# Performance work log

Hardware: AMD Instinct MI355X
Metric: run time of the kernel (lower is better)

Reference implementation:

```python
import jax, jax.numpy as jnp
import numpy as np

TOP_K = 2


def setup_inputs() -> dict:
    key = jax.random.key(0)
    ks = jax.random.split(key, 5)
    B, S, D, F, E = 2, 2048, 1024, 3584, 8
    scale_in = 1.0 / np.sqrt(D)
    scale_f = 1.0 / np.sqrt(F)
    return {
        "hidden_states": jax.random.normal(ks[0], (B, S, D), dtype=jnp.float32),
        "gate_w": jax.random.normal(ks[1], (E, D), dtype=jnp.float32) * scale_in,
        "w1": jax.random.normal(ks[2], (E, F, D), dtype=jnp.float32) * scale_in,
        "w3": jax.random.normal(ks[3], (E, F, D), dtype=jnp.float32) * scale_in,
        "w2": jax.random.normal(ks[4], (E, D, F), dtype=jnp.float32) * scale_f,
    }


def _routing_weights(logits):
    # softmax over experts, select top-k, renormalize (Mixtral semantics)
    probs = jax.nn.softmax(logits, axis=-1)          # [T, E]
    topv, topi = jax.lax.top_k(probs, TOP_K)          # [T, k]
    topv = topv / jnp.sum(topv, axis=-1, keepdims=True)
    T, E = logits.shape
    w = jnp.zeros((T, E), dtype=logits.dtype)
    w = w.at[jnp.arange(T)[:, None], topi].set(topv)  # dense [T, E] routing weights
    return w


def reference(hidden_states, gate_w, w1, w3, w2):
    B, S, D = hidden_states.shape
    x = hidden_states.reshape(-1, D)                  # [T, D]
    logits = x @ gate_w.T                             # [T, E]
    rw = _routing_weights(logits)                     # [T, E]
    E = gate_w.shape[0]
    out = jnp.zeros_like(x)
    for e in range(E):                                # fixed small expert count
        h = jax.nn.silu(x @ w1[e].T) * (x @ w3[e].T)  # [T, F]
        out = out + rw[:, e:e + 1] * (h @ w2[e].T)    # [T, D]
    return out.reshape(B, S, D)
```

## Files before the change

kernel.cpp:

```cpp
#include <hip/hip_runtime.h>
#include <hip/hip_bf16.h>


#define T_TOK 4096
#define DIM   1024
#define FF    3584
#define NE    8
#define CAP   (T_TOK*2 + NE*256)

#define OFF_TOPI   256UL
#define OFF_TOPW   33024UL
#define OFF_ROWTOK 65792UL
#define OFF_ROWW   106752UL
#define OFF_W1B    147712UL
#define OFF_W3B    (OFF_W1B + 58720256UL)
#define OFF_W2B    OFF_W1B
#define OFF_H      (OFF_W1B + 117440512UL)
#define WS_NEED    (OFF_H + 73400320UL)

using f32x4 = __attribute__((ext_vector_type(4))) float;
using s16x8 = __attribute__((ext_vector_type(8))) short;

__device__ __forceinline__ ushort f2b(float f) {
    __hip_bfloat16 b = __float2bfloat16(f);
    ushort u; __builtin_memcpy(&u, &b, 2); return u;
}
__device__ __forceinline__ void gl_lds16(const ushort* g, ushort* l) {
    __builtin_amdgcn_global_load_lds(
        (const __attribute__((address_space(1))) void*)g,
        (__attribute__((address_space(3))) void*)l, 16, 0, 0);
}
__device__ __forceinline__ uint4 pack8(float4 v0, float4 v1) {
    uint4 o;
    o.x = f2b(v0.x) | ((uint)f2b(v0.y) << 16);
    o.y = f2b(v0.z) | ((uint)f2b(v0.w) << 16);
    o.z = f2b(v1.x) | ((uint)f2b(v1.y) << 16);
    o.w = f2b(v1.z) | ((uint)f2b(v1.w) << 16);
    return o;
}

#define LGKM0 do { asm volatile("s_waitcnt lgkmcnt(0)" ::: "memory"); \
                   __builtin_amdgcn_sched_barrier(0); } while (0)
#define VMC(n) asm volatile("s_waitcnt vmcnt(" #n ")" ::: "memory")
#define BAR()  __builtin_amdgcn_s_barrier()

__global__ __launch_bounds__(256)
void k_route(const float* __restrict__ x, const float* __restrict__ gw,
             int* __restrict__ topi, float* __restrict__ topw,
             int* __restrict__ counts, ushort* __restrict__ xb)
{
    __shared__ float gws[NE*DIM];
    const int tid = threadIdx.x;
    for (int i = tid; i < NE*DIM/4; i += 256)
        ((float4*)gws)[i] = ((const float4*)gw)[i];
    __syncthreads();

    const int lane = tid & 63, wid = tid >> 6;
    const int t = blockIdx.x*4 + wid;

    float4 xr[4];
    const float4* xrow = (const float4*)(x + (size_t)t*DIM) + lane*4;
    #pragma unroll
    for (int i = 0; i < 4; ++i) xr[i] = xrow[i];

    uint4* xbd = (uint4*)(xb + (size_t)t*DIM);
    xbd[lane*2]   = pack8(xr[0], xr[1]);
    xbd[lane*2+1] = pack8(xr[2], xr[3]);

    float lg[NE];
    #pragma unroll
    for (int e = 0; e < NE; ++e) {
        const float4* g4 = (const float4*)(gws + e*DIM) + lane*4;
        float s = 0.f;
        #pragma unroll
        for (int i = 0; i < 4; ++i) {
            float4 g = g4[i];
            s += xr[i].x*g.x + xr[i].y*g.y + xr[i].z*g.z + xr[i].w*g.w;
        }
        #pragma unroll
        for (int off = 32; off; off >>= 1) s += __shfl_xor(s, off);
        lg[e] = s;
    }
    if (lane == 0) {
        float b1 = -1e30f, b2 = -1e30f; int i1 = 0, i2 = 0;
        #pragma unroll
        for (int e = 0; e < NE; ++e) {
            float v = lg[e];
            if (v > b1)      { b2 = b1; i2 = i1; b1 = v; i1 = e; }
            else if (v > b2) { b2 = v; i2 = e; }
        }
        float p2 = __expf(b2 - b1);
        float inv = 1.f / (1.f + p2);
        topi[2*t]   = i1; topi[2*t+1] = i2;
        topw[2*t]   = inv; topw[2*t+1] = p2*inv;
        atomicAdd(&counts[i1], 1); atomicAdd(&counts[i2], 1);
    }
}

__global__ void k_scan(const int* __restrict__ counts, int* __restrict__ offs,
                       int* __restrict__ rowTok)
{
    if (threadIdx.x == 0) {
        int acc = 0; offs[0] = 0;
        for (int e = 0; e < NE; ++e) {
            int p = (counts[e] + 255) & ~255;
            acc += p; offs[e+1] = acc;
        }
    }
    for (int i = threadIdx.x; i < CAP; i += blockDim.x) rowTok[i] = -1;
}

__global__ __launch_bounds__(256)
void k_scatter(const int* __restrict__ topi, const float* __restrict__ topw,
               const int* __restrict__ offs, int* __restrict__ cursor,
               int* __restrict__ rowTok, float* __restrict__ rowW)
{
    int t = blockIdx.x*256 + threadIdx.x;
    #pragma unroll
    for (int j = 0; j < 2; ++j) {
        int e = topi[2*t + j];
        int pos = offs[e] + atomicAdd(&cursor[e], 1);
        rowTok[pos] = t;
        rowW[pos] = topw[2*t + j];
    }
}

__global__ __launch_bounds__(256)
void k_cvt(const float* __restrict__ src, ushort* __restrict__ dst)
{
    size_t i = (size_t)blockIdx.x*256 + threadIdx.x;
    float4 v0 = ((const float4*)src)[2*i], v1 = ((const float4*)src)[2*i+1];
    ((uint4*)dst)[i] = pack8(v0, v1);
}

#define G1_SLOT 12288
__global__ __launch_bounds__(256, 2)
void k_gemm1(const ushort* __restrict__ xb,
             const ushort* __restrict__ w1b, const ushort* __restrict__ w3b,
             const int* __restrict__ offs, const int* __restrict__ rowTok,
             ushort* __restrict__ hout)
{
    __shared__ __align__(16) ushort L[3*G1_SLOT];
    const int sb = blockIdx.x;
    const int rowStart = blockIdx.y * 256;
    if (rowStart >= offs[8]) return;
    int e = 0;
    #pragma unroll
    for (int k = 1; k < NE; ++k) if (rowStart >= offs[k]) e = k;

    const int tid = threadIdx.x, lane = tid & 63, wid = tid >> 6;
    const int wr = wid >> 1, wc = wid & 1;
    const int lo = lane & 15, hi = lane >> 4;

    const int srow = lane >> 2;
    const int sch  = (lane & 3) ^ ((lane >> 3) & 3);
    const ushort* aS[4];
    #pragma unroll
    for (int j = 0; j < 4; ++j) {
        int tk = rowTok[rowStart + j*64 + wid*16 + srow]; if (tk < 0) tk = 0;
        aS[j] = xb + (size_t)tk*DIM + sch*8;
    }
    const ushort* bS[2];
    bS[0] = w1b + ((size_t)e*FF + sb*64 + wid*16 + srow)*DIM + sch*8;
    bS[1] = w3b + ((size_t)e*FF + sb*64 + wid*16 + srow)*DIM + sch*8;
    ushort* const dA = L + wid*512;
    ushort* const dB = L + 8192 + wid*512;

    const int sig = (lo >> 1) & 3;
    const int roff = ((hi ^ sig) * 8);
    int rdA[8], rdB[4];
    #pragma unroll
    for (int m = 0; m < 8; ++m) rdA[m] = (wr*128 + m*16 + lo)*32 + roff;
    #pragma unroll
    for (int n = 0; n < 2; ++n) {
        rdB[n]   = 8192 + (wc*32 + n*16 + lo)*32 + roff;
        rdB[n+2] = 8192 + (64 + wc*32 + n*16 + lo)*32 + roff;
    }

    f32x4 acc[8][4];
    #pragma unroll
    for (int m = 0; m < 8; ++m)
        #pragma unroll
        for (int n = 0; n < 4; ++n) acc[m][n] = (f32x4)(0.f);

    #pragma unroll
    for (int t0 = 0; t0 < 2; ++t0) {
        #pragma unroll
        for (int j = 0; j < 4; ++j) gl_lds16(aS[j] + t0*32, dA + t0*G1_SLOT + j*2048);
        #pragma unroll
        for (int j = 0; j < 2; ++j) gl_lds16(bS[j] + t0*32, dB + t0*G1_SLOT + j*2048);
    }
    VMC(6);
    BAR();

    const int NK = DIM/32;
    int cur = 0, nxt = 2;
    for (int t = 0; t < NK; ++t) {
        const ushort* Lb = L + cur*G1_SLOT;
        const bool pf = (t + 2 < NK);
        s16x8 a[4], b[4];
        #pragma unroll
        for (int n = 0; n < 4; ++n) b[n] = *(const s16x8*)(Lb + rdB[n]);
        #pragma unroll
        for (int m = 0; m < 4; ++m) a[m] = *(const s16x8*)(Lb + rdA[m]);
        if (pf) {
            #pragma unroll
            for (int j = 0; j < 3; ++j)
                gl_lds16(aS[j] + (t+2)*32, dA + nxt*G1_SLOT + j*2048);
        }
        BAR();
        LGKM0;
        __builtin_amdgcn_s_setprio(1);
        #pragma unroll
        for (int m = 0; m < 4; ++m)
            #pragma unroll
            for (int n = 0; n < 4; ++n)
                acc[m][n] = __builtin_amdgcn_mfma_f32_16x16x32_bf16(a[m], b[n], acc[m][n], 0, 0, 0);
        __builtin_amdgcn_s_setprio(0);
        BAR();
        #pragma unroll
        for (int m = 0; m < 4; ++m) a[m] = *(const s16x8*)(Lb + rdA[4+m]);
        if (pf) {
            gl_lds16(aS[3] + (t+2)*32, dA + nxt*G1_SLOT + 3*2048);
            gl_lds16(bS[0] + (t+2)*32, dB + nxt*G1_SLOT);
            gl_lds16(bS[1] + (t+2)*32, dB + nxt*G1_SLOT + 2048);
        }
        BAR();
        LGKM0;
        __builtin_amdgcn_s_setprio(1);
        #pragma unroll
        for (int m = 0; m < 4; ++m)
            #pragma unroll
            for (int n = 0; n < 4; ++n)
                acc[4+m][n] = __builtin_amdgcn_mfma_f32_16x16x32_bf16(a[m], b[n], acc[4+m][n], 0, 0, 0);
        __builtin_amdgcn_s_setprio(0);
        if (t < NK-2) { VMC(6); } else { VMC(0); }
        BAR();
        cur = (cur == 2) ? 0 : cur + 1;
        nxt = (nxt == 2) ? 0 : nxt + 1;
    }

    #pragma unroll
    for (int m = 0; m < 8; ++m)
        #pragma unroll
        for (int p = 0; p < 2; ++p) {
            f32x4 v1 = acc[m][p], v3 = acc[m][p+2];
            int f = sb*64 + wc*32 + p*16 + lo;
            #pragma unroll
            for (int j = 0; j < 4; ++j) {
                int row = rowStart + wr*128 + m*16 + hi*4 + j;
                float s = v1[j];
                float val = (s / (1.f + __expf(-s))) * v3[j];
                hout[(size_t)row*FF + f] = f2b(val);
            }
        }
}

#define G2S 8192
__global__ __launch_bounds__(128)
void k_gemm2(const ushort* __restrict__ h, const ushort* __restrict__ w2b,
             const int* __restrict__ offs, const int* __restrict__ rowTok,
             const float* __restrict__ rowW, float* __restrict__ out)
{
    __shared__ __align__(16) ushort L[3*G2S];
    const int dc = blockIdx.x * 128;
    const int rowStart = blockIdx.y * 128;
    if (rowStart >= offs[8]) return;
    int e = 0;
    #pragma unroll
    for (int k = 1; k < NE; ++k) if (rowStart >= offs[k]) e = k;

    const int tid = threadIdx.x, lane = tid & 63, w = tid >> 6;
    const int lo = lane & 15, hi = lane >> 4;

    const int srow = lane >> 2;
    const int sch  = (lane & 3) ^ ((lane >> 3) & 3);
    const ushort* aS[4]; const ushort* bS[4];
    #pragma unroll
    for (int j = 0; j < 4; ++j) {
        int r = j*32 + w*16 + srow;
        aS[j] = h   + (size_t)(rowStart + r)*FF + sch*8;
        bS[j] = w2b + ((size_t)e*DIM + dc + r)*FF + sch*8;
    }

    const int sig = (lo >> 1) & 3;
    const int roff = ((hi ^ sig) * 8);
    int rdA[4], rdB[8];
    #pragma unroll
    for (int m = 0; m < 4; ++m) rdA[m] = (w*64 + m*16 + lo)*32 + roff;
    #pragma unroll
    for (int n = 0; n < 8; ++n) rdB[n] = 4096 + (n*16 + lo)*32 + roff;

    f32x4 acc[4][8];
    #pragma unroll
    for (int m = 0; m < 4; ++m)
        #pragma unroll
        for (int n = 0; n < 8; ++n) acc[m][n] = (f32x4)(0.f);

    #pragma unroll
    for (int t0 = 0; t0 < 2; ++t0) {
        #pragma unroll
        for (int j = 0; j < 4; ++j) gl_lds16(aS[j] + t0*32, L + t0*G2S + j*1024 + w*512);
        #pragma unroll
        for (int j = 0; j < 4; ++j) gl_lds16(bS[j] + t0*32, L + t0*G2S + 4096 + j*1024 + w*512);
    }
    VMC(8);
    BAR();

    const int NK = FF/32;
    int cur = 0, nxt = 2;
    for (int t = 0; t < NK; ++t) {
        const ushort* Lb = L + cur*G2S;
        ushort* Ln = L + nxt*G2S;
        const bool pf = (t + 2 < NK);
        s16x8 a[4], b[8];
        #pragma unroll
        for (int n = 0; n < 8; ++n) b[n] = *(const s16x8*)(Lb + rdB[n]);
        #pragma unroll
        for (int m = 0; m < 4; ++m) a[m] = *(const s16x8*)(Lb + rdA[m]);
        if (pf) {
            #pragma unroll
            for (int j = 0; j < 4; ++j) gl_lds16(aS[j] + (t+2)*32, Ln + j*1024 + w*512);
            #pragma unroll
            for (int j = 0; j < 4; ++j) gl_lds16(bS[j] + (t+2)*32, Ln + 4096 + j*1024 + w*512);
        }
        BAR();
        LGKM0;
        __builtin_amdgcn_s_setprio(1);
        #pragma unroll
        for (int m = 0; m < 4; ++m)
            #pragma unroll
            for (int n = 0; n < 8; ++n)
                acc[m][n] = __builtin_amdgcn_mfma_f32_16x16x32_bf16(a[m], b[n], acc[m][n], 0, 0, 0);
        __builtin_amdgcn_s_setprio(0);
        if (t < NK-2) { VMC(8); } else { VMC(0); }
        BAR();
        cur = (cur == 2) ? 0 : cur + 1;
        nxt = (nxt == 2) ? 0 : nxt + 1;
    }

    #pragma unroll
    for (int m = 0; m < 4; ++m)
        #pragma unroll
        for (int j = 0; j < 4; ++j) {
            int prow = rowStart + w*64 + m*16 + hi*4 + j;
            int tok = rowTok[prow];
            if (tok < 0) continue;
            float wgt = rowW[prow];
            #pragma unroll
            for (int n = 0; n < 8; ++n) {
                int d = dc + n*16 + lo;
                atomicAdd(&out[(size_t)tok*DIM + d], wgt * acc[m][n][j]);
            }
        }
}

extern "C" void kernel_launch(void* const* d_in, const int* in_sizes, int n_in,
                              void* d_out, int out_size, void* d_ws, size_t ws_size,
                              hipStream_t stream)
{
    const float* x  = (const float*)d_in[0];
    const float* gw = (const float*)d_in[1];
    const float* w1 = (const float*)d_in[2];
    const float* w3 = (const float*)d_in[3];
    const float* w2 = (const float*)d_in[4];
    float* out = (float*)d_out;
    char* ws = (char*)d_ws;
    if (ws_size < WS_NEED) return;

    int*    counts = (int*)ws;
    int*    cursor = counts + 8;
    int*    offs   = counts + 16;
    int*    topi   = (int*)  (ws + OFF_TOPI);
    float*  topw   = (float*)(ws + OFF_TOPW);
    int*    rowTok = (int*)  (ws + OFF_ROWTOK);
    float*  rowW   = (float*)(ws + OFF_ROWW);
    ushort* w1b    = (ushort*)(ws + OFF_W1B);
    ushort* w3b    = (ushort*)(ws + OFF_W3B);
    ushort* w2b    = (ushort*)(ws + OFF_W2B);
    ushort* h      = (ushort*)(ws + OFF_H);
    ushort* xb     = (ushort*)d_out;

    hipMemsetAsync(ws, 0, 256, stream);

    k_route  <<<T_TOK/4, 256, 0, stream>>>(x, gw, topi, topw, counts, xb);
    k_scan   <<<1, 256, 0, stream>>>(counts, offs, rowTok);
    k_scatter<<<T_TOK/256, 256, 0, stream>>>(topi, topw, offs, cursor, rowTok, rowW);
    k_cvt    <<<(NE*FF*DIM/8)/256, 256, 0, stream>>>(w1, w1b);
    k_cvt    <<<(NE*FF*DIM/8)/256, 256, 0, stream>>>(w3, w3b);
    k_gemm1  <<<dim3(56, CAP/256), 256, 0, stream>>>(xb, w1b, w3b, offs, rowTok, h);
    k_cvt    <<<(NE*DIM*FF/8)/256, 256, 0, stream>>>(w2, w2b);
    hipMemsetAsync(d_out, 0, (size_t)T_TOK*DIM*4, stream);
    k_gemm2  <<<dim3(DIM/128, CAP/128), 128, 0, stream>>>(h, w2b, offs, rowTok, rowW, out);
}
```

Baseline: 539.3 us.

## Retile expert down-projection GEMM to 256x128 with split-K over two halves

The second grouped GEMM now uses 256-thread blocks computing 256x128 output tiles, reusing the first GEMM's LDS slot layout. The F reduction is split in two halves across blockIdx.z, and partial sums are combined through the existing atomic adds into the output. Each K step is broken into two MFMA phases, with A-fragment loads and global-to-LDS prefetches interleaved between them. The aim is better operand reuse per block and more parallelism, at the cost of twice as many atomic adds and extra barriers per step.

```diff
diff --git a/kernel.cpp b/kernel.cpp
--- a/kernel.cpp
+++ b/kernel.cpp
@@ -256,73 +256,75 @@
         }
 }
 
-#define G2S 8192
-__global__ __launch_bounds__(128)
+__global__ __launch_bounds__(256, 2)
 void k_gemm2(const ushort* __restrict__ h, const ushort* __restrict__ w2b,
              const int* __restrict__ offs, const int* __restrict__ rowTok,
              const float* __restrict__ rowW, float* __restrict__ out)
 {
-    __shared__ __align__(16) ushort L[3*G2S];
+    __shared__ __align__(16) ushort L[3*G1_SLOT];
     const int dc = blockIdx.x * 128;
-    const int rowStart = blockIdx.y * 128;
+    const int rowStart = blockIdx.y * 256;
     if (rowStart >= offs[8]) return;
     int e = 0;
     #pragma unroll
     for (int k = 1; k < NE; ++k) if (rowStart >= offs[k]) e = k;
-
-    const int tid = threadIdx.x, lane = tid & 63, w = tid >> 6;
+    const int kbase = blockIdx.z * (FF/2);
+
+    const int tid = threadIdx.x, lane = tid & 63, wid = tid >> 6;
+    const int wr = wid >> 1, wc = wid & 1;
     const int lo = lane & 15, hi = lane >> 4;
 
     const int srow = lane >> 2;
     const int sch  = (lane & 3) ^ ((lane >> 3) & 3);
-    const ushort* aS[4]; const ushort* bS[4];
-    #pragma unroll
-    for (int j = 0; j < 4; ++j) {
-        int r = j*32 + w*16 + srow;
-        aS[j] = h   + (size_t)(rowStart + r)*FF + sch*8;
-        bS[j] = w2b + ((size_t)e*DIM + dc + r)*FF + sch*8;
-    }
+    const ushort* aS[4];
+    #pragma unroll
+    for (int j = 0; j < 4; ++j)
+        aS[j] = h + (size_t)(rowStart + j*64 + wid*16 + srow)*FF + kbase + sch*8;
+    const ushort* bS[2];
+    #pragma unroll
+    for (int j = 0; j < 2; ++j)
+        bS[j] = w2b + ((size_t)e*DIM + dc + j*64 + wid*16 + srow)*FF + kbase + sch*8;
+    ushort* const dA = L + wid*512;
+    ushort* const dB = L + 8192 + wid*512;
 
     const int sig = (lo >> 1) & 3;
     const int roff = ((hi ^ sig) * 8);
-    int rdA[4], rdB[8];
-    #pragma unroll
-    for (int m = 0; m < 4; ++m) rdA[m] = (w*64 + m*16 + lo)*32 + roff;
-    #pragma unroll
-    for (int n = 0; n < 8; ++n) rdB[n] = 4096 + (n*16 + lo)*32 + roff;
-
-    f32x4 acc[4][8];
-    #pragma unroll
-    for (int m = 0; m < 4; ++m)
-        #pragma unroll
-        for (int n = 0; n < 8; ++n) acc[m][n] = (f32x4)(0.f);
+    int rdA[8], rdB[4];
+    #pragma unroll
+    for (int m = 0; m < 8; ++m) rdA[m] = (wr*128 + m*16 + lo)*32 + roff;
+    #pragma unroll
+    for (int n = 0; n < 4; ++n) rdB[n] = 8192 + (wc*64 + n*16 + lo)*32 + roff;
+
+    f32x4 acc[8][4];
+    #pragma unroll
+    for (int m = 0; m < 8; ++m)
+        #pragma unroll
+        for (int n = 0; n < 4; ++n) acc[m][n] = (f32x4)(0.f);
 
     #pragma unroll
     for (int t0 = 0; t0 < 2; ++t0) {
         #pragma unroll
-        for (int j = 0; j < 4; ++j) gl_lds16(aS[j] + t0*32, L + t0*G2S + j*1024 + w*512);
-        #pragma unroll
-        for (int j = 0; j < 4; ++j) gl_lds16(bS[j] + t0*32, L + t0*G2S + 4096 + j*1024 + w*512);
-    }
-    VMC(8);
+        for (int j = 0; j < 4; ++j) gl_lds16(aS[j] + t0*32, dA + t0*G1_SLOT + j*2048);
+        #pragma unroll
+        for (int j = 0; j < 2; ++j) gl_lds16(bS[j] + t0*32, dB + t0*G1_SLOT + j*2048);
+    }
+    VMC(6);
     BAR();
 
-    const int NK = FF/32;
+    const int NK = (FF/2)/32;
     int cur = 0, nxt = 2;
     for (int t = 0; t < NK; ++t) {
-        const ushort* Lb = L + cur*G2S;
-        ushort* Ln = L + nxt*G2S;
+        const ushort* Lb = L + cur*G1_SLOT;
         const bool pf = (t + 2 < NK);
-        s16x8 a[4], b[8];
-        #pragma unroll
-        for (int n = 0; n < 8; ++n) b[n] = *(const s16x8*)(Lb + rdB[n]);
+        s16x8 a[4], b[4];
+        #pragma unroll
+        for (int n = 0; n < 4; ++n) b[n] = *(const s16x8*)(Lb + rdB[n]);
         #pragma unroll
         for (int m = 0; m < 4; ++m) a[m] = *(const s16x8*)(Lb + rdA[m]);
         if (pf) {
             #pragma unroll
-            for (int j = 0; j < 4; ++j) gl_lds16(aS[j] + (t+2)*32, Ln + j*1024 + w*512);
-            #pragma unroll
-            for (int j = 0; j < 4; ++j) gl_lds16(bS[j] + (t+2)*32, Ln + 4096 + j*1024 + w*512);
+            for (int j = 0; j < 3; ++j)
+                gl_lds16(aS[j] + (t+2)*32, dA + nxt*G1_SLOT + j*2048);
         }
         BAR();
         LGKM0;
@@ -330,27 +332,44 @@
         #pragma unroll
         for (int m = 0; m < 4; ++m)
             #pragma unroll
-            for (int n = 0; n < 8; ++n)
+            for (int n = 0; n < 4; ++n)
                 acc[m][n] = __builtin_amdgcn_mfma_f32_16x16x32_bf16(a[m], b[n], acc[m][n], 0, 0, 0);
         __builtin_amdgcn_s_setprio(0);
-        if (t < NK-2) { VMC(8); } else { VMC(0); }
+        BAR();
+        #pragma unroll
+        for (int m = 0; m < 4; ++m) a[m] = *(const s16x8*)(Lb + rdA[4+m]);
+        if (pf) {
+            gl_lds16(aS[3] + (t+2)*32, dA + nxt*G1_SLOT + 3*2048);
+            gl_lds16(bS[0] + (t+2)*32, dB + nxt*G1_SLOT);
+            gl_lds16(bS[1] + (t+2)*32, dB + nxt*G1_SLOT + 2048);
+        }
+        BAR();
+        LGKM0;
+        __builtin_amdgcn_s_setprio(1);
+        #pragma unroll
+        for (int m = 0; m < 4; ++m)
+            #pragma unroll
+            for (int n = 0; n < 4; ++n)
+                acc[4+m][n] = __builtin_amdgcn_mfma_f32_16x16x32_bf16(a[m], b[n], acc[4+m][n], 0, 0, 0);
+        __builtin_amdgcn_s_setprio(0);
+        if (t < NK-2) { VMC(6); } else { VMC(0); }
         BAR();
         cur = (cur == 2) ? 0 : cur + 1;
         nxt = (nxt == 2) ? 0 : nxt + 1;
     }
 
     #pragma unroll
-    for (int m = 0; m < 4; ++m)
+    for (int m = 0; m < 8; ++m)
         #pragma unroll
         for (int j = 0; j < 4; ++j) {
-            int prow = rowStart + w*64 + m*16 + hi*4 + j;
+            int prow = rowStart + wr*128 + m*16 + hi*4 + j;
             int tok = rowTok[prow];
             if (tok < 0) continue;
-            float wgt = rowW[prow];
-            #pragma unroll
-            for (int n = 0; n < 8; ++n) {
-                int d = dc + n*16 + lo;
-                atomicAdd(&out[(size_t)tok*DIM + d], wgt * acc[m][n][j]);
+            float w = rowW[prow];
+            #pragma unroll
+            for (int n = 0; n < 4; ++n) {
+                int d = dc + wc*64 + n*16 + lo;
+                atomicAdd(&out[(size_t)tok*DIM + d], w * acc[m][n][j]);
             }
         }
 }
@@ -391,5 +410,5 @@
     k_gemm1  <<<dim3(56, CAP/256), 256, 0, stream>>>(xb, w1b, w3b, offs, rowTok, h);
     k_cvt    <<<(NE*DIM*FF/8)/256, 256, 0, stream>>>(w2, w2b);
     hipMemsetAsync(d_out, 0, (size_t)T_TOK*DIM*4, stream);
-    k_gemm2  <<<dim3(DIM/128, CAP/128), 128, 0, stream>>>(h, w2b, offs, rowTok, rowW, out);
-}
+    k_gemm2  <<<dim3(8, CAP/256, 2), 256, 0, stream>>>(h, w2b, offs, rowTok, rowW, out);
+}
```

After: 533.9 us. About the same (-1.0%).
